# Optimization experiments

Hardware: AMD Instinct MI355X
Metric: run time of the kernel (lower is better)

Reference implementation:

```python
import jax, jax.numpy as jnp
import numpy as np

B, T, D, NH, L, E, K = 2, 1024, 512, 8, 4, 8, 2
H = D * 4
HD = D // NH
EPS = 1e-5
THETA = 10000.0
MOE_LAYERS = (0, 2)   # layer_idx % moe_freq == 0
DENSE_LAYERS = (1, 3)


def setup_inputs() -> dict:
    key = jax.random.key(0)
    ks = jax.random.split(key, 12)
    s = 0.02
    return {
        "x": jax.random.normal(ks[0], (B, T, D), jnp.float32),
        "qkv_w": jax.random.normal(ks[1], (L, 3 * D, D), jnp.float32) * s,
        "out_w": jax.random.normal(ks[2], (L, D, D), jnp.float32) * s,
        "norm1_w": jnp.ones((L, D), jnp.float32),
        "norm2_w": jnp.ones((L, D), jnp.float32),
        "router_w": jax.random.normal(ks[3], (2, E, D), jnp.float32) * s,
        "moe_w1": jax.random.normal(ks[4], (2, E, H, D), jnp.float32) * s,
        "moe_w2": jax.random.normal(ks[5], (2, E, D, H), jnp.float32) * s,
        "moe_w3": jax.random.normal(ks[6], (2, E, H, D), jnp.float32) * s,
        "f_w1": jax.random.normal(ks[7], (2, H, D), jnp.float32) * s,
        "f_w2": jax.random.normal(ks[8], (2, D, H), jnp.float32) * s,
        "f_w3": jax.random.normal(ks[9], (2, H, D), jnp.float32) * s,
        "norm_f": jnp.ones((D,), jnp.float32),
    }


def rmsnorm(x, w):
    return w * x * jax.lax.rsqrt(jnp.mean(x * x, axis=-1, keepdims=True) + EPS)


def rope_tables():
    inv_freq = 1.0 / (THETA ** (jnp.arange(0, HD, 2, dtype=jnp.float32) / HD))  # [HD/2]
    t = jnp.arange(T, dtype=jnp.float32)
    freqs = t[:, None] * inv_freq[None, :]  # [T, HD/2]
    return jnp.cos(freqs), jnp.sin(freqs)


def apply_rope(x, cos, sin):  # x: [B, NH, T, HD]
    x1, x2 = jnp.split(x, 2, axis=-1)
    return jnp.concatenate([x1 * cos - x2 * sin, x1 * sin + x2 * cos], axis=-1)


def attention(x, qkv_w, out_w, cos, sin, causal):
    qkv = x @ qkv_w.T  # [B, T, 3D]
    q, k, v = jnp.split(qkv, 3, axis=-1)
    sh = lambda a: a.reshape(B, T, NH, HD).transpose(0, 2, 1, 3)  # [B, NH, T, HD]
    q, k, v = sh(q), sh(k), sh(v)
    q = apply_rope(q, cos, sin)
    k = apply_rope(k, cos, sin)
    scores = jnp.einsum('bhqd,bhkd->bhqk', q, k) / np.sqrt(HD).astype(np.float32)
    scores = jnp.where(causal, scores, jnp.finfo(scores.dtype).min)
    attn = jax.nn.softmax(scores, axis=-1)
    out = jnp.einsum('bhqk,bhkd->bhqd', attn, v)
    out = out.transpose(0, 2, 1, 3).reshape(B, T, D)
    return out @ out_w.T


def swiglu(x, w1, w2, w3):
    return (jax.nn.silu(x @ w1.T) * (x @ w3.T)) @ w2.T


def moe(x, rw, w1, w2, w3):  # x: [N, D]
    n = x.shape[0]
    logits = x @ rw.T                              # [N, E]
    top_v, top_i = jax.lax.top_k(logits, K)        # [N, K]
    wts = jax.nn.softmax(top_v, axis=-1)           # [N, K]
    # combine[t, e] = sum_i wts[t, i] * 1[top_i[t, i] == e]
    combine = jnp.zeros((n, E), x.dtype).at[jnp.arange(n)[:, None], top_i].add(wts)
    gate = jax.nn.silu(jnp.einsum('nd,ehd->neh', x, w1))
    up = jnp.einsum('nd,ehd->neh', x, w3)
    expert_out = jnp.einsum('neh,edh->ned', gate * up, w2)  # [N, E, D]
    return jnp.einsum('ne,ned->nd', combine, expert_out)


def reference(x, qkv_w, out_w, norm1_w, norm2_w, router_w, moe_w1, moe_w2,
              moe_w3, f_w1, f_w2, f_w3, norm_f):
    cos, sin = rope_tables()
    causal = jnp.tril(jnp.ones((T, T), bool))
    h = x
    for l in range(L):
        h = h + attention(rmsnorm(h, norm1_w[l]), qkv_w[l], out_w[l], cos, sin, causal)
        hn = rmsnorm(h, norm2_w[l])
        if l in MOE_LAYERS:
            m = MOE_LAYERS.index(l)
            ff = moe(hn.reshape(-1, D), router_w[m], moe_w1[m], moe_w2[m], moe_w3[m]).reshape(B, T, D)
        else:
            m = DENSE_LAYERS.index(l)
            ff = swiglu(hn, f_w1[m], f_w2[m], f_w3[m])
        h = h + ff
    return rmsnorm(h, norm_f)
```

## Files before the change

### kernel.cpp

```cpp
#include <hip/hip_runtime.h>
#include <hip/hip_bf16.h>
#include <math.h>

#define Bc 2
#define Tc 1024
#define Dc 512
#define NHc 8
#define Lc 4
#define Ec 8
#define Kc 2
#define Hc 2048
#define HDc 64
#define Nc (Bc * Tc)
#define NKc (Nc * Kc)

typedef __bf16 bf16x8 __attribute__((ext_vector_type(8)));
typedef float  f32x4  __attribute__((ext_vector_type(4)));
typedef unsigned short ushort8v __attribute__((ext_vector_type(8)));

__device__ inline unsigned short f2bf(float f) {
    union { float f; unsigned u; } v; v.f = f;
    unsigned r = v.u + 0x7FFFu + ((v.u >> 16) & 1u);
    return (unsigned short)(r >> 16);
}
__device__ inline float bf2f(unsigned short b) {
    union { unsigned u; float f; } v; v.u = ((unsigned)b) << 16;
    return v.f;
}
__device__ inline void splitbf(float a, unsigned short& hi, unsigned short& lo) {
    unsigned short h = f2bf(a);
    hi = h;
    lo = f2bf(a - bf2f(h));
}
__device__ inline void split8(const float4& a, const float4& b,
                              ushort8v& h, ushort8v& l) {
    unsigned short hh, ll;
    splitbf(a.x, hh, ll); h[0] = hh; l[0] = ll;
    splitbf(a.y, hh, ll); h[1] = hh; l[1] = ll;
    splitbf(a.z, hh, ll); h[2] = hh; l[2] = ll;
    splitbf(a.w, hh, ll); h[3] = hh; l[3] = ll;
    splitbf(b.x, hh, ll); h[4] = hh; l[4] = ll;
    splitbf(b.y, hh, ll); h[5] = hh; l[5] = ll;
    splitbf(b.z, hh, ll); h[6] = hh; l[6] = ll;
    splitbf(b.w, hh, ll); h[7] = hh; l[7] = ll;
}

__global__ __launch_bounds__(256) void rmsnorm_kernel(
    const float* __restrict__ x, const float* __restrict__ w,
    float* __restrict__ y)
{
    int row = blockIdx.x;
    const float* xr = x + (size_t)row * Dc;
    __shared__ float red[256];
    int tid = threadIdx.x;
    float ss = 0.0f;
    for (int d = tid; d < Dc; d += 256) { float v = xr[d]; ss += v * v; }
    red[tid] = ss; __syncthreads();
    for (int s = 128; s > 0; s >>= 1) {
        if (tid < s) red[tid] += red[tid + s];
        __syncthreads();
    }
    float inv = rsqrtf(red[0] / (float)Dc + 1e-5f);
    for (int d = tid; d < Dc; d += 256)
        y[(size_t)row * Dc + d] = w[d] * xr[d] * inv;
}

template<int MODE, int TM, int TN>
__global__ __launch_bounds__(256) void gemm3(
    const float* __restrict__ A, const float* __restrict__ Wbase,
    float* __restrict__ C, int M, int N, int K,
    const int* __restrict__ tok, const float* __restrict__ twt,
    const int* __restrict__ counts, const int* __restrict__ offsets,
    size_t wstride)
{
    constexpr int PAD = 40;
    constexpr int PA  = TM / 64;
    constexpr int PB  = TN / 64;
    constexpr int FM  = TM / 32;
    constexpr int FN  = TN / 32;

    int e = (MODE == 5) ? blockIdx.z : 0;
    int count = M, offs = 0;
    if (MODE == 5) {
        count = counts[e];
        offs  = offsets[e];
        if ((int)(blockIdx.y * TM) >= count) return;
    }
    const float* W = Wbase + (size_t)e * wstride;

    __shared__ __align__(16) unsigned short Ah[TM][PAD];
    __shared__ __align__(16) unsigned short Al[TM][PAD];
    __shared__ __align__(16) unsigned short Bh[TN][PAD];
    __shared__ __align__(16) unsigned short Bl[TN][PAD];

    int tid = threadIdx.x;
    int m0 = blockIdx.y * TM, n0 = blockIdx.x * TN;
    int srow = tid >> 2;
    int scol = (tid & 3) * 8;

    int wave = tid >> 6, lane = tid & 63;
    int wm = wave >> 1, wn = wave & 1;
    int quad = lane >> 4, l16 = lane & 15;

    f32x4 acc[FM][FN];
#pragma unroll
    for (int mi = 0; mi < FM; ++mi)
#pragma unroll
        for (int ni = 0; ni < FN; ++ni)
            acc[mi][ni] = (f32x4){0.f, 0.f, 0.f, 0.f};

    size_t arow[PA];
#pragma unroll
    for (int p = 0; p < PA; ++p) {
        int row = p * 64 + srow;
        if (MODE == 5) {
            int rr = m0 + row; if (rr >= count) rr = 0;
            arow[p] = (size_t)(offs + rr) * K;
        } else {
            arow[p] = (size_t)(m0 + row) * K;
        }
    }
    size_t brow[PB];
#pragma unroll
    for (int p = 0; p < PB; ++p)
        brow[p] = (size_t)(n0 + p * 64 + srow) * K;

    float4 pa[PA][2], pb[PB][2];
#pragma unroll
    for (int p = 0; p < PA; ++p) {
        pa[p][0] = *(const float4*)(A + arow[p] + scol);
        pa[p][1] = *(const float4*)(A + arow[p] + scol + 4);
    }
#pragma unroll
    for (int p = 0; p < PB; ++p) {
        pb[p][0] = *(const float4*)(W + brow[p] + scol);
        pb[p][1] = *(const float4*)(W + brow[p] + scol + 4);
    }

    for (int k0 = 0; k0 < K; k0 += 32) {
#pragma unroll
        for (int p = 0; p < PA; ++p) {
            int row = p * 64 + srow;
            ushort8v h, l;
            split8(pa[p][0], pa[p][1], h, l);
            *(ushort8v*)&Ah[row][scol] = h;
            *(ushort8v*)&Al[row][scol] = l;
        }
#pragma unroll
        for (int p = 0; p < PB; ++p) {
            int row = p * 64 + srow;
            ushort8v h, l;
            split8(pb[p][0], pb[p][1], h, l);
            *(ushort8v*)&Bh[row][scol] = h;
            *(ushort8v*)&Bl[row][scol] = l;
        }
        __syncthreads();
        if (k0 + 32 < K) {
            int kn = k0 + 32;
#pragma unroll
            for (int p = 0; p < PA; ++p) {
                pa[p][0] = *(const float4*)(A + arow[p] + kn + scol);
                pa[p][1] = *(const float4*)(A + arow[p] + kn + scol + 4);
            }
#pragma unroll
            for (int p = 0; p < PB; ++p) {
                pb[p][0] = *(const float4*)(W + brow[p] + kn + scol);
                pb[p][1] = *(const float4*)(W + brow[p] + kn + scol + 4);
            }
        }

        bf16x8 ah[FM], al[FM], bh[FN], bl[FN];
#pragma unroll
        for (int mi = 0; mi < FM; ++mi) {
            ah[mi] = *(const bf16x8*)&Ah[wm * (TM / 2) + mi * 16 + l16][quad * 8];
            al[mi] = *(const bf16x8*)&Al[wm * (TM / 2) + mi * 16 + l16][quad * 8];
        }
#pragma unroll
        for (int ni = 0; ni < FN; ++ni) {
            bh[ni] = *(const bf16x8*)&Bh[wn * (TN / 2) + ni * 16 + l16][quad * 8];
            bl[ni] = *(const bf16x8*)&Bl[wn * (TN / 2) + ni * 16 + l16][quad * 8];
        }
#pragma unroll
        for (int mi = 0; mi < FM; ++mi)
#pragma unroll
            for (int ni = 0; ni < FN; ++ni) {
                acc[mi][ni] = __builtin_amdgcn_mfma_f32_16x16x32_bf16(
                    ah[mi], bh[ni], acc[mi][ni], 0, 0, 0);
                acc[mi][ni] = __builtin_amdgcn_mfma_f32_16x16x32_bf16(
                    al[mi], bh[ni], acc[mi][ni], 0, 0, 0);
                acc[mi][ni] = __builtin_amdgcn_mfma_f32_16x16x32_bf16(
                    ah[mi], bl[ni], acc[mi][ni], 0, 0, 0);
            }
        __syncthreads();
    }

#pragma unroll
    for (int mi = 0; mi < FM; ++mi) {
#pragma unroll
        for (int ni = 0; ni < FN; ++ni) {
            int col = n0 + wn * (TN / 2) + ni * 16 + l16;
#pragma unroll
            for (int r = 0; r < 4; ++r) {
                int row = wm * (TM / 2) + mi * 16 + quad * 4 + r;
                float v = acc[mi][ni][r];
                if (MODE == 0) {
                    C[(size_t)(m0 + row) * N + col] = v;
                } else if (MODE == 1) {
                    C[(size_t)(m0 + row) * N + col] += v;
                } else {
                    int rr = m0 + row;
                    if (rr < count) {
                        int dest = tok[offs + rr];
                        float w = twt[offs + rr];
                        atomicAdd(&C[(size_t)dest * N + col], w * v);
                    }
                }
            }
        }
    }
}

template<bool GATHER>
__global__ __launch_bounds__(256) void ffn_fused(
    const float* __restrict__ A, const float* __restrict__ W1base,
    const float* __restrict__ W3base, float* __restrict__ T,
    int M, int N, int K,
    const int* __restrict__ tok, const int* __restrict__ counts,
    const int* __restrict__ offsets, size_t wstride)
{
    constexpr int TM = 64, TN = 128, PAD = 40;
    constexpr int FM = 2, FN = 4;

    int e = GATHER ? blockIdx.z : 0;
    int count = M, offs = 0;
    if (GATHER) {
        count = counts[e];
        offs  = offsets[e];
        if ((int)(blockIdx.y * TM) >= count) return;
    }
    const float* W1 = W1base + (size_t)e * wstride;
    const float* W3 = W3base + (size_t)e * wstride;

    __shared__ __align__(16) unsigned short Ah[TM][PAD];
    __shared__ __align__(16) unsigned short Al[TM][PAD];
    __shared__ __align__(16) unsigned short B1h[TN][PAD];
    __shared__ __align__(16) unsigned short B1l[TN][PAD];
    __shared__ __align__(16) unsigned short B3h[TN][PAD];
    __shared__ __align__(16) unsigned short B3l[TN][PAD];
    __shared__ int sTok[TM];

    int tid = threadIdx.x;
    int m0 = blockIdx.y * TM, n0 = blockIdx.x * TN;

    if (GATHER) {
        if (tid < TM) {
            int r = m0 + tid;
            sTok[tid] = (r < count) ? tok[offs + r] : tok[offs];
        }
        __syncthreads();
    }

    int srow = tid >> 2;
    int scol = (tid & 3) * 8;
    int wave = tid >> 6, lane = tid & 63;
    int wm = wave >> 1, wn = wave & 1;
    int quad = lane >> 4, l16 = lane & 15;

    f32x4 accg[FM][FN], accu[FM][FN];
#pragma unroll
    for (int mi = 0; mi < FM; ++mi)
#pragma unroll
        for (int ni = 0; ni < FN; ++ni) {
            accg[mi][ni] = (f32x4){0.f, 0.f, 0.f, 0.f};
            accu[mi][ni] = (f32x4){0.f, 0.f, 0.f, 0.f};
        }

    size_t arow;
    if (GATHER) arow = (size_t)sTok[srow] * K;
    else        arow = (size_t)(m0 + srow) * K;
    size_t brow[2];
    brow[0] = (size_t)(n0 + srow) * K;
    brow[1] = (size_t)(n0 + 64 + srow) * K;

    float4 pa[2], p1[2][2], p3[2][2];
    pa[0] = *(const float4*)(A + arow + scol);
    pa[1] = *(const float4*)(A + arow + scol + 4);
#pragma unroll
    for (int p = 0; p < 2; ++p) {
        p1[p][0] = *(const float4*)(W1 + brow[p] + scol);
        p1[p][1] = *(const float4*)(W1 + brow[p] + scol + 4);
        p3[p][0] = *(const float4*)(W3 + brow[p] + scol);
        p3[p][1] = *(const float4*)(W3 + brow[p] + scol + 4);
    }

    for (int k0 = 0; k0 < K; k0 += 32) {
        {
            ushort8v h, l;
            split8(pa[0], pa[1], h, l);
            *(ushort8v*)&Ah[srow][scol] = h;
            *(ushort8v*)&Al[srow][scol] = l;
        }
#pragma unroll
        for (int p = 0; p < 2; ++p) {
            int row = p * 64 + srow;
            ushort8v h, l;
            split8(p1[p][0], p1[p][1], h, l);
            *(ushort8v*)&B1h[row][scol] = h;
            *(ushort8v*)&B1l[row][scol] = l;
            split8(p3[p][0], p3[p][1], h, l);
            *(ushort8v*)&B3h[row][scol] = h;
            *(ushort8v*)&B3l[row][scol] = l;
        }
        __syncthreads();
        if (k0 + 32 < K) {
            int kn = k0 + 32;
            pa[0] = *(const float4*)(A + arow + kn + scol);
            pa[1] = *(const float4*)(A + arow + kn + scol + 4);
#pragma unroll
            for (int p = 0; p < 2; ++p) {
                p1[p][0] = *(const float4*)(W1 + brow[p] + kn + scol);
                p1[p][1] = *(const float4*)(W1 + brow[p] + kn + scol + 4);
                p3[p][0] = *(const float4*)(W3 + brow[p] + kn + scol);
                p3[p][1] = *(const float4*)(W3 + brow[p] + kn + scol + 4);
            }
        }

        bf16x8 ah[FM], al[FM], bh[FN], bl[FN];
#pragma unroll
        for (int mi = 0; mi < FM; ++mi) {
            ah[mi] = *(const bf16x8*)&Ah[wm * 32 + mi * 16 + l16][quad * 8];
            al[mi] = *(const bf16x8*)&Al[wm * 32 + mi * 16 + l16][quad * 8];
        }
#pragma unroll
        for (int ni = 0; ni < FN; ++ni) {
            bh[ni] = *(const bf16x8*)&B1h[wn * 64 + ni * 16 + l16][quad * 8];
            bl[ni] = *(const bf16x8*)&B1l[wn * 64 + ni * 16 + l16][quad * 8];
        }
#pragma unroll
        for (int mi = 0; mi < FM; ++mi)
#pragma unroll
            for (int ni = 0; ni < FN; ++ni) {
                accg[mi][ni] = __builtin_amdgcn_mfma_f32_16x16x32_bf16(
                    ah[mi], bh[ni], accg[mi][ni], 0, 0, 0);
                accg[mi][ni] = __builtin_amdgcn_mfma_f32_16x16x32_bf16(
                    al[mi], bh[ni], accg[mi][ni], 0, 0, 0);
                accg[mi][ni] = __builtin_amdgcn_mfma_f32_16x16x32_bf16(
                    ah[mi], bl[ni], accg[mi][ni], 0, 0, 0);
            }
#pragma unroll
        for (int ni = 0; ni < FN; ++ni) {
            bh[ni] = *(const bf16x8*)&B3h[wn * 64 + ni * 16 + l16][quad * 8];
            bl[ni] = *(const bf16x8*)&B3l[wn * 64 + ni * 16 + l16][quad * 8];
        }
#pragma unroll
        for (int mi = 0; mi < FM; ++mi)
#pragma unroll
            for (int ni = 0; ni < FN; ++ni) {
                accu[mi][ni] = __builtin_amdgcn_mfma_f32_16x16x32_bf16(
                    ah[mi], bh[ni], accu[mi][ni], 0, 0, 0);
                accu[mi][ni] = __builtin_amdgcn_mfma_f32_16x16x32_bf16(
                    al[mi], bh[ni], accu[mi][ni], 0, 0, 0);
                accu[mi][ni] = __builtin_amdgcn_mfma_f32_16x16x32_bf16(
                    ah[mi], bl[ni], accu[mi][ni], 0, 0, 0);
            }
        __syncthreads();
    }

#pragma unroll
    for (int mi = 0; mi < FM; ++mi) {
#pragma unroll
        for (int ni = 0; ni < FN; ++ni) {
            int col = n0 + wn * 64 + ni * 16 + l16;
#pragma unroll
            for (int r = 0; r < 4; ++r) {
                int row = wm * 32 + mi * 16 + quad * 4 + r;
                float g = accg[mi][ni][r];
                float u = accu[mi][ni][r];
                float t = (g / (1.0f + expf(-g))) * u;
                if (GATHER) {
                    int rr = m0 + row;
                    if (rr < count) T[(size_t)(offs + rr) * N + col] = t;
                } else {
                    T[(size_t)(m0 + row) * N + col] = t;
                }
            }
        }
    }
}

__global__ __launch_bounds__(256) void rope_kernel(float* __restrict__ qkv)
{
    const int HD2 = HDc / 2;
    int idx = blockIdx.x * blockDim.x + threadIdx.x;
    int total = Nc * NHc * HD2;
    if (idx >= total) return;
    int i = idx % HD2;
    int hh = (idx / HD2) % NHc;
    int n = idx / (HD2 * NHc);
    int t = n % Tc;
    float invf = expf(-(2.0f * (float)i / (float)HDc) * logf(10000.0f));
    float f = (float)t * invf;
    float c = cosf(f), s = sinf(f);
    size_t base = (size_t)n * (3 * Dc) + (size_t)hh * HDc;
    float* qp = qkv + base;
    float* kp = qkv + base + Dc;
    float q1 = qp[i], q2 = qp[i + HD2];
    qp[i]       = q1 * c - q2 * s;
    qp[i + HD2] = q1 * s + q2 * c;
    float k1 = kp[i], k2 = kp[i + HD2];
    kp[i]       = k1 * c - k2 * s;
    kp[i + HD2] = k1 * s + k2 * c;
}

__global__ __launch_bounds__(256) void attn_mfma(
    const float* __restrict__ qkv, float* __restrict__ out)
{
    constexpr int PAD = 72;
    __shared__ __align__(16) unsigned short Qh[64][PAD];
    __shared__ __align__(16) unsigned short Ql[64][PAD];
    __shared__ __align__(16) unsigned short Kh[64][PAD];
    __shared__ __align__(16) unsigned short Kl[64][PAD];
    __shared__ __align__(16) unsigned short Vth[64][PAD];
    __shared__ __align__(16) unsigned short Vtl[64][PAD];

    int qb = blockIdx.x, bh = blockIdx.y;
    int b = bh >> 3, hh = bh & 7;
    const int D3 = 3 * Dc;
    const float* base = qkv + (size_t)b * Tc * D3 + (size_t)hh * HDc;

    int tid = threadIdx.x;
    int wave = tid >> 6, lane = tid & 63;
    int quad = lane >> 4, l16 = lane & 15;

    int srow = tid >> 2;
    int scb  = (tid & 3) * 16;
    int vhd  = lane;
    int vkb  = wave * 16;

    {
        const float* qp = base + (size_t)(qb * 64 + srow) * D3 + scb;
        float4 q0 = *(const float4*)(qp);
        float4 q1 = *(const float4*)(qp + 4);
        float4 q2 = *(const float4*)(qp + 8);
        float4 q3 = *(const float4*)(qp + 12);
        const float sc = 0.125f;
        q0.x *= sc; q0.y *= sc; q0.z *= sc; q0.w *= sc;
        q1.x *= sc; q1.y *= sc; q1.z *= sc; q1.w *= sc;
        q2.x *= sc; q2.y *= sc; q2.z *= sc; q2.w *= sc;
        q3.x *= sc; q3.y *= sc; q3.z *= sc; q3.w *= sc;
        ushort8v h, l;
        split8(q0, q1, h, l);
        *(ushort8v*)&Qh[srow][scb]     = h;
        *(ushort8v*)&Ql[srow][scb]     = l;
        split8(q2, q3, h, l);
        *(ushort8v*)&Qh[srow][scb + 8] = h;
        *(ushort8v*)&Ql[srow][scb + 8] = l;
    }
    __syncthreads();
    bf16x8 qah[2], qal[2];
#pragma unroll
    for (int ks = 0; ks < 2; ++ks) {
        qah[ks] = *(const bf16x8*)&Qh[wave * 16 + l16][ks * 32 + quad * 8];
        qal[ks] = *(const bf16x8*)&Ql[wave * 16 + l16][ks * 32 + quad * 8];
    }

    float4 kf0, kf1, kf2, kf3;
    float vf[16];
    {
        const float* kp = base + (size_t)srow * D3 + Dc + scb;
        kf0 = *(const float4*)(kp);
        kf1 = *(const float4*)(kp + 4);
        kf2 = *(const float4*)(kp + 8);
        kf3 = *(const float4*)(kp + 12);
        const float* vp = base + (size_t)vkb * D3 + 2 * Dc + vhd;
#pragma unroll
        for (int i = 0; i < 16; ++i) vf[i] = vp[(size_t)i * D3];
    }

    f32x4 o[4];
#pragma unroll
    for (int f = 0; f < 4; ++f) o[f] = (f32x4){0.f, 0.f, 0.f, 0.f};
    float mrow[4], lrow[4];
#pragma unroll
    for (int r = 0; r < 4; ++r) { mrow[r] = -1e30f; lrow[r] = 0.0f; }

    for (int kt = 0; kt <= qb; ++kt) {
        __syncthreads();
        {
            ushort8v h, l;
            split8(kf0, kf1, h, l);
            *(ushort8v*)&Kh[srow][scb]     = h;
            *(ushort8v*)&Kl[srow][scb]     = l;
            split8(kf2, kf3, h, l);
            *(ushort8v*)&Kh[srow][scb + 8] = h;
            *(ushort8v*)&Kl[srow][scb + 8] = l;
        }
        {
            float4 v0 = make_float4(vf[0], vf[1], vf[2], vf[3]);
            float4 v1 = make_float4(vf[4], vf[5], vf[6], vf[7]);
            float4 v2 = make_float4(vf[8], vf[9], vf[10], vf[11]);
            float4 v3 = make_float4(vf[12], vf[13], vf[14], vf[15]);
            ushort8v h, l;
            split8(v0, v1, h, l);
            *(ushort8v*)&Vth[vhd][vkb]     = h;
            *(ushort8v*)&Vtl[vhd][vkb]     = l;
            split8(v2, v3, h, l);
            *(ushort8v*)&Vth[vhd][vkb + 8] = h;
            *(ushort8v*)&Vtl[vhd][vkb + 8] = l;
        }
        __syncthreads();
        if (kt < qb) {
            const float* kp = base + (size_t)((kt + 1) * 64 + srow) * D3 + Dc + scb;
            kf0 = *(const float4*)(kp);
            kf1 = *(const float4*)(kp + 4);
            kf2 = *(const float4*)(kp + 8);
            kf3 = *(const float4*)(kp + 12);
            const float* vp = base + (size_t)((kt + 1) * 64 + vkb) * D3 + 2 * Dc + vhd;
#pragma unroll
            for (int i = 0; i < 16; ++i) vf[i] = vp[(size_t)i * D3];
        }

        f32x4 s[4];
#pragma unroll
        for (int ni = 0; ni < 4; ++ni) s[ni] = (f32x4){0.f, 0.f, 0.f, 0.f};
#pragma unroll
        for (int ks = 0; ks < 2; ++ks) {
            bf16x8 kh_[4], kl_[4];
#pragma unroll
            for (int ni = 0; ni < 4; ++ni) {
                kh_[ni] = *(const bf16x8*)&Kh[ni * 16 + l16][ks * 32 + quad * 8];
                kl_[ni] = *(const bf16x8*)&Kl[ni * 16 + l16][ks * 32 + quad * 8];
            }
#pragma unroll
            for (int ni = 0; ni < 4; ++ni) {
                s[ni] = __builtin_amdgcn_mfma_f32_16x16x32_bf16(
                    qah[ks], kh_[ni], s[ni], 0, 0, 0);
                s[ni] = __builtin_amdgcn_mfma_f32_16x16x32_bf16(
                    qal[ks], kh_[ni], s[ni], 0, 0, 0);
                s[ni] = __builtin_amdgcn_mfma_f32_16x16x32_bf16(
                    qah[ks], kl_[ni], s[ni], 0, 0, 0);
            }
        }

        if (kt == qb) {
#pragma unroll
            for (int ni = 0; ni < 4; ++ni)
#pragma unroll
                for (int r = 0; r < 4; ++r)
                    if (ni * 16 + l16 > wave * 16 + quad * 4 + r)
                        s[ni][r] = -1e30f;
        }

        float al4[4];
#pragma unroll
        for (int r = 0; r < 4; ++r) {
            float rm = fmaxf(fmaxf(s[0][r], s[1][r]), fmaxf(s[2][r], s[3][r]));
            rm = fmaxf(rm, __shfl_xor(rm, 1));
            rm = fmaxf(rm, __shfl_xor(rm, 2));
            rm = fmaxf(rm, __shfl_xor(rm, 4));
            rm = fmaxf(rm, __shfl_xor(rm, 8));
            float mn = fmaxf(mrow[r], rm);
            al4[r] = __expf(mrow[r] - mn);
            mrow[r] = mn;
            float rs = 0.0f;
#pragma unroll
            for (int ni = 0; ni < 4; ++ni) {
                float pv = __expf(s[ni][r] - mn);
                s[ni][r] = pv;
                rs += pv;
            }
            rs += __shfl_xor(rs, 1);
            rs += __shfl_xor(rs, 2);
            rs += __shfl_xor(rs, 4);
            rs += __shfl_xor(rs, 8);
            lrow[r] = lrow[r] * al4[r] + rs;
        }

        __syncthreads();
#pragma unroll
        for (int ni = 0; ni < 4; ++ni)
#pragma unroll
            for (int r = 0; r < 4; ++r) {
                unsigned short hp, lp;
                splitbf(s[ni][r], hp, lp);
                Kh[wave * 16 + quad * 4 + r][ni * 16 + l16] = hp;
                Kl[wave * 16 + quad * 4 + r][ni * 16 + l16] = lp;
            }
#pragma unroll
        for (int f = 0; f < 4; ++f)
#pragma unroll
            for (int r = 0; r < 4; ++r)
                o[f][r] *= al4[r];
#pragma unroll
        for (int ks = 0; ks < 2; ++ks) {
            bf16x8 pah = *(const bf16x8*)&Kh[wave * 16 + l16][ks * 32 + quad * 8];
            bf16x8 pal = *(const bf16x8*)&Kl[wave * 16 + l16][ks * 32 + quad * 8];
#pragma unroll
            for (int f = 0; f < 4; ++f) {
                bf16x8 vh_ = *(const bf16x8*)&Vth[f * 16 + l16][ks * 32 + quad * 8];
                bf16x8 vl_ = *(const bf16x8*)&Vtl[f * 16 + l16][ks * 32 + quad * 8];
                o[f] = __builtin_amdgcn_mfma_f32_16x16x32_bf16(
                    pah, vh_, o[f], 0, 0, 0);
                o[f] = __builtin_amdgcn_mfma_f32_16x16x32_bf16(
                    pal, vh_, o[f], 0, 0, 0);
                o[f] = __builtin_amdgcn_mfma_f32_16x16x32_bf16(
                    pah, vl_, o[f], 0, 0, 0);
            }
        }
    }

#pragma unroll
    for (int r = 0; r < 4; ++r) {
        float inv = 1.0f / lrow[r];
        int q = qb * 64 + wave * 16 + quad * 4 + r;
#pragma unroll
        for (int f = 0; f < 4; ++f)
            out[(size_t)(b * Tc + q) * Dc + hh * HDc + f * 16 + l16] =
                o[f][r] * inv;
    }
}

__global__ __launch_bounds__(64) void router_kernel(
    const float* __restrict__ x, const float* __restrict__ rw,
    float* __restrict__ logits)
{
    int n = blockIdx.x;
    int lane = threadIdx.x;
    const float* xr = x + (size_t)n * Dc;
    for (int e = 0; e < Ec; ++e) {
        const float* wr = rw + (size_t)e * Dc;
        float p = 0.0f;
        for (int d = lane; d < Dc; d += 64) p += xr[d] * wr[d];
        for (int off = 32; off > 0; off >>= 1) p += __shfl_down(p, off);
        if (lane == 0) logits[(size_t)n * Ec + e] = p;
    }
}

__global__ void zero8_kernel(int* __restrict__ counts)
{
    if (threadIdx.x < Ec) counts[threadIdx.x] = 0;
}

__global__ __launch_bounds__(256) void topk_count_kernel(
    const float* __restrict__ logits, int* __restrict__ counts,
    int2* __restrict__ eidx, float2* __restrict__ ewt)
{
    int n = blockIdx.x * blockDim.x + threadIdx.x;
    if (n >= Nc) return;
    const float* lg = logits + (size_t)n * Ec;
    int i0 = -1, i1 = -1;
    float v0 = -1e30f, v1 = -1e30f;
    for (int e = 0; e < Ec; ++e) {
        float v = lg[e];
        if (v > v0) { v1 = v0; i1 = i0; v0 = v; i0 = e; }
        else if (v > v1) { v1 = v; i1 = e; }
    }
    float e1 = expf(v1 - v0);
    float w0 = 1.0f / (1.0f + e1);
    float w1 = e1 / (1.0f + e1);
    atomicAdd(&counts[i0], 1);
    atomicAdd(&counts[i1], 1);
    eidx[n] = make_int2(i0, i1);
    ewt[n]  = make_float2(w0, w1);
}

__global__ void scan_kernel(int* __restrict__ counts, int* __restrict__ offsets)
{
    if (threadIdx.x == 0) {
        int s = 0;
        for (int e = 0; e < Ec; ++e) { offsets[e] = s; s += counts[e]; counts[e] = 0; }
    }
}

__global__ __launch_bounds__(256) void topk_place_kernel(
    const int2* __restrict__ eidx, const float2* __restrict__ ewt,
    int* __restrict__ counts, const int* __restrict__ offsets,
    int* __restrict__ tok, float* __restrict__ twt)
{
    int n = blockIdx.x * blockDim.x + threadIdx.x;
    if (n >= Nc) return;
    int2 ei = eidx[n];
    float2 w = ewt[n];
    int p0 = atomicAdd(&counts[ei.x], 1);
    int r0 = offsets[ei.x] + p0;
    tok[r0] = n; twt[r0] = w.x;
    int p1 = atomicAdd(&counts[ei.y], 1);
    int r1 = offsets[ei.y] + p1;
    tok[r1] = n; twt[r1] = w.y;
}

extern "C" void kernel_launch(void* const* d_in, const int* in_sizes, int n_in,
                              void* d_out, int out_size, void* d_ws, size_t ws_size,
                              hipStream_t stream)
{
    const float* x        = (const float*)d_in[0];
    const float* qkv_w    = (const float*)d_in[1];
    const float* out_w    = (const float*)d_in[2];
    const float* norm1_w  = (const float*)d_in[3];
    const float* norm2_w  = (const float*)d_in[4];
    const float* router_w = (const float*)d_in[5];
    const float* moe_w1   = (const float*)d_in[6];
    const float* moe_w2   = (const float*)d_in[7];
    const float* moe_w3   = (const float*)d_in[8];
    const float* f_w1     = (const float*)d_in[9];
    const float* f_w2     = (const float*)d_in[10];
    const float* f_w3     = (const float*)d_in[11];
    const float* norm_f   = (const float*)d_in[12];
    float* out = (float*)d_out;

    float* p = (float*)d_ws;
    float* h      = p;  p += Nc * Dc;
    float* xn     = p;  p += Nc * Dc;
    float* arena  = p;  p += (size_t)NKc * Hc;
    float* logits = p;  p += Nc * Ec;
    int*   counts  = (int*)p;  p += 16;
    int*   offsets = (int*)p;  p += 16;
    int2*  eidx    = (int2*)p; p += 2 * Nc;
    float* ewt     = p;        p += 2 * Nc;
    int*   tok     = (int*)p;  p += NKc;
    float* twt     = p;        p += NKc;

    float* qkv  = arena;
    float* attn = xn;
    float* t    = arena;

    hipMemcpyAsync(h, x, (size_t)Nc * Dc * sizeof(float),
                   hipMemcpyDeviceToDevice, stream);

    for (int l = 0; l < Lc; ++l) {
        rmsnorm_kernel<<<Nc, 256, 0, stream>>>(h, norm1_w + (size_t)l * Dc, xn);
        gemm3<0, 64, 128><<<dim3(3 * Dc / 128, Nc / 64, 1), 256, 0, stream>>>(
            xn, qkv_w + (size_t)l * 3 * Dc * Dc, qkv, Nc, 3 * Dc, Dc,
            nullptr, nullptr, nullptr, nullptr, 0);
        {
            int total = Nc * NHc * (HDc / 2);
            rope_kernel<<<(total + 255) / 256, 256, 0, stream>>>(qkv);
        }
        attn_mfma<<<dim3(Tc / 64, Bc * NHc), 256, 0, stream>>>(qkv, attn);
        gemm3<1, 64, 64><<<dim3(Dc / 64, Nc / 64, 1), 256, 0, stream>>>(
            attn, out_w + (size_t)l * Dc * Dc, h, Nc, Dc, Dc,
            nullptr, nullptr, nullptr, nullptr, 0);

        rmsnorm_kernel<<<Nc, 256, 0, stream>>>(h, norm2_w + (size_t)l * Dc, xn);
        if (l == 0 || l == 2) {
            int m = l / 2;
            router_kernel<<<Nc, 64, 0, stream>>>(
                xn, router_w + (size_t)m * Ec * Dc, logits);
            zero8_kernel<<<1, 64, 0, stream>>>(counts);
            topk_count_kernel<<<Nc / 256, 256, 0, stream>>>(
                logits, counts, eidx, (float2*)ewt);
            scan_kernel<<<1, 64, 0, stream>>>(counts, offsets);
            topk_place_kernel<<<Nc / 256, 256, 0, stream>>>(
                eidx, (float2*)ewt, counts, offsets, tok, twt);

            ffn_fused<true><<<dim3(Hc / 128, NKc / 64, Ec), 256, 0, stream>>>(
                xn, moe_w1 + (size_t)m * Ec * Hc * Dc,
                moe_w3 + (size_t)m * Ec * Hc * Dc, t, Nc, Hc, Dc,
                tok, counts, offsets, (size_t)Hc * Dc);
            gemm3<5, 64, 64><<<dim3(Dc / 64, NKc / 64, Ec), 256, 0, stream>>>(
                t, moe_w2 + (size_t)m * Ec * Dc * Hc, h, Nc, Dc, Hc,
                tok, twt, counts, offsets, (size_t)Dc * Hc);
        } else {
            int m = (l - 1) / 2;
            ffn_fused<false><<<dim3(Hc / 128, Nc / 64, 1), 256, 0, stream>>>(
                xn, f_w1 + (size_t)m * Hc * Dc, f_w3 + (size_t)m * Hc * Dc,
                t, Nc, Hc, Dc, nullptr, nullptr, nullptr, 0);
            gemm3<1, 64, 64><<<dim3(Dc / 64, Nc / 64, 1), 256, 0, stream>>>(
                t, f_w2 + (size_t)m * Dc * Hc, h, Nc, Dc, Hc,
                nullptr, nullptr, nullptr, nullptr, 0);
        }
    }

    rmsnorm_kernel<<<Nc, 256, 0, stream>>>(h, norm_f, out);
}
```

Baseline: 1.413 ms.

## Pre-split weights and activations into bf16 hi/lo arrays before GEMMs

Adds a split_w kernel that converts each fp32 weight matrix into separate bf16 hi and lo arrays before use. The rmsnorm, attention and FFN epilogues now also write their outputs as hi/lo bf16 pairs. The GEMM kernels then load the pre-split operands directly instead of converting fp32 tiles inside the k-loop. This removes redundant per-tile split arithmetic, which was repeated across every block that reads the same tile, at the cost of extra launches and an extra full pass over all weights on every call.

```diff
diff --git a/kernel.cpp b/kernel.cpp
--- a/kernel.cpp
+++ b/kernel.cpp
@@ -17,6 +17,7 @@
 typedef __bf16 bf16x8 __attribute__((ext_vector_type(8)));
 typedef float  f32x4  __attribute__((ext_vector_type(4)));
 typedef unsigned short ushort8v __attribute__((ext_vector_type(8)));
+typedef unsigned short ushort4v __attribute__((ext_vector_type(4)));
 
 __device__ inline unsigned short f2bf(float f) {
     union { float f; unsigned u; } v; v.f = f;
@@ -45,9 +46,27 @@
     splitbf(b.w, hh, ll); h[7] = hh; l[7] = ll;
 }
 
-__global__ __launch_bounds__(256) void rmsnorm_kernel(
+__global__ __launch_bounds__(256) void split_w_kernel(
+    const float* __restrict__ w, unsigned short* __restrict__ hi,
+    unsigned short* __restrict__ lo, int n4)
+{
+    int i = blockIdx.x * 256 + threadIdx.x;
+    if (i >= n4) return;
+    float4 v = ((const float4*)w)[i];
+    ushort4v h, l;
+    unsigned short a, b;
+    splitbf(v.x, a, b); h[0] = a; l[0] = b;
+    splitbf(v.y, a, b); h[1] = a; l[1] = b;
+    splitbf(v.z, a, b); h[2] = a; l[2] = b;
+    splitbf(v.w, a, b); h[3] = a; l[3] = b;
+    ((ushort4v*)hi)[i] = h;
+    ((ushort4v*)lo)[i] = l;
+}
+
+__global__ __launch_bounds__(256) void rmsnorm_split_kernel(
     const float* __restrict__ x, const float* __restrict__ w,
-    float* __restrict__ y)
+    float* __restrict__ y, unsigned short* __restrict__ yh,
+    unsigned short* __restrict__ yl)
 {
     int row = blockIdx.x;
     const float* xr = x + (size_t)row * Dc;
@@ -61,13 +80,40 @@
         __syncthreads();
     }
     float inv = rsqrtf(red[0] / (float)Dc + 1e-5f);
+    for (int d = tid; d < Dc; d += 256) {
+        float v = w[d] * xr[d] * inv;
+        size_t idx = (size_t)row * Dc + d;
+        y[idx] = v;
+        unsigned short h, l;
+        splitbf(v, h, l);
+        yh[idx] = h; yl[idx] = l;
+    }
+}
+
+__global__ __launch_bounds__(256) void rmsnorm_kernel(
+    const float* __restrict__ x, const float* __restrict__ w,
+    float* __restrict__ y)
+{
+    int row = blockIdx.x;
+    const float* xr = x + (size_t)row * Dc;
+    __shared__ float red[256];
+    int tid = threadIdx.x;
+    float ss = 0.0f;
+    for (int d = tid; d < Dc; d += 256) { float v = xr[d]; ss += v * v; }
+    red[tid] = ss; __syncthreads();
+    for (int s = 128; s > 0; s >>= 1) {
+        if (tid < s) red[tid] += red[tid + s];
+        __syncthreads();
+    }
+    float inv = rsqrtf(red[0] / (float)Dc + 1e-5f);
     for (int d = tid; d < Dc; d += 256)
         y[(size_t)row * Dc + d] = w[d] * xr[d] * inv;
 }
 
 template<int MODE, int TM, int TN>
-__global__ __launch_bounds__(256) void gemm3(
-    const float* __restrict__ A, const float* __restrict__ Wbase,
+__global__ __launch_bounds__(256) void gemm3p(
+    const unsigned short* __restrict__ Ahi, const unsigned short* __restrict__ Alo,
+    const unsigned short* __restrict__ Whibase, const unsigned short* __restrict__ Wlobase,
     float* __restrict__ C, int M, int N, int K,
     const int* __restrict__ tok, const float* __restrict__ twt,
     const int* __restrict__ counts, const int* __restrict__ offsets,
@@ -86,7 +132,8 @@
         offs  = offsets[e];
         if ((int)(blockIdx.y * TM) >= count) return;
     }
-    const float* W = Wbase + (size_t)e * wstride;
+    const unsigned short* Whi = Whibase + (size_t)e * wstride;
+    const unsigned short* Wlo = Wlobase + (size_t)e * wstride;
 
     __shared__ __align__(16) unsigned short Ah[TM][PAD];
     __shared__ __align__(16) unsigned short Al[TM][PAD];
@@ -125,47 +172,43 @@
     for (int p = 0; p < PB; ++p)
         brow[p] = (size_t)(n0 + p * 64 + srow) * K;
 
-    float4 pa[PA][2], pb[PB][2];
+    ushort8v pah[PA], pal[PA], pbh[PB], pbl[PB];
 #pragma unroll
     for (int p = 0; p < PA; ++p) {
-        pa[p][0] = *(const float4*)(A + arow[p] + scol);
-        pa[p][1] = *(const float4*)(A + arow[p] + scol + 4);
+        pah[p] = *(const ushort8v*)(Ahi + arow[p] + scol);
+        pal[p] = *(const ushort8v*)(Alo + arow[p] + scol);
     }
 #pragma unroll
     for (int p = 0; p < PB; ++p) {
-        pb[p][0] = *(const float4*)(W + brow[p] + scol);
-        pb[p][1] = *(const float4*)(W + brow[p] + scol + 4);
+        pbh[p] = *(const ushort8v*)(Whi + brow[p] + scol);
+        pbl[p] = *(const ushort8v*)(Wlo + brow[p] + scol);
     }
 
     for (int k0 = 0; k0 < K; k0 += 32) {
 #pragma unroll
         for (int p = 0; p < PA; ++p) {
             int row = p * 64 + srow;
-            ushort8v h, l;
-            split8(pa[p][0], pa[p][1], h, l);
-            *(ushort8v*)&Ah[row][scol] = h;
-            *(ushort8v*)&Al[row][scol] = l;
+            *(ushort8v*)&Ah[row][scol] = pah[p];
+            *(ushort8v*)&Al[row][scol] = pal[p];
         }
 #pragma unroll
         for (int p = 0; p < PB; ++p) {
             int row = p * 64 + srow;
-            ushort8v h, l;
-            split8(pb[p][0], pb[p][1], h, l);
-            *(ushort8v*)&Bh[row][scol] = h;
-            *(ushort8v*)&Bl[row][scol] = l;
+            *(ushort8v*)&Bh[row][scol] = pbh[p];
+            *(ushort8v*)&Bl[row][scol] = pbl[p];
         }
         __syncthreads();
         if (k0 + 32 < K) {
             int kn = k0 + 32;
 #pragma unroll
             for (int p = 0; p < PA; ++p) {
-                pa[p][0] = *(const float4*)(A + arow[p] + kn + scol);
-                pa[p][1] = *(const float4*)(A + arow[p] + kn + scol + 4);
+                pah[p] = *(const ushort8v*)(Ahi + arow[p] + kn + scol);
+                pal[p] = *(const ushort8v*)(Alo + arow[p] + kn + scol);
             }
 #pragma unroll
             for (int p = 0; p < PB; ++p) {
-                pb[p][0] = *(const float4*)(W + brow[p] + kn + scol);
-                pb[p][1] = *(const float4*)(W + brow[p] + kn + scol + 4);
+                pbh[p] = *(const ushort8v*)(Whi + brow[p] + kn + scol);
+                pbl[p] = *(const ushort8v*)(Wlo + brow[p] + kn + scol);
             }
         }
 
@@ -221,9 +264,11 @@
 }
 
 template<bool GATHER>
-__global__ __launch_bounds__(256) void ffn_fused(
-    const float* __restrict__ A, const float* __restrict__ W1base,
-    const float* __restrict__ W3base, float* __restrict__ T,
+__global__ __launch_bounds__(256) void ffn_fusedp(
+    const unsigned short* __restrict__ Ahi, const unsigned short* __restrict__ Alo,
+    const unsigned short* __restrict__ W1hibase, const unsigned short* __restrict__ W1lobase,
+    const unsigned short* __restrict__ W3hibase, const unsigned short* __restrict__ W3lobase,
+    unsigned short* __restrict__ Thi, unsigned short* __restrict__ Tlo,
     int M, int N, int K,
     const int* __restrict__ tok, const int* __restrict__ counts,
     const int* __restrict__ offsets, size_t wstride)
@@ -238,8 +283,10 @@
         offs  = offsets[e];
         if ((int)(blockIdx.y * TM) >= count) return;
     }
-    const float* W1 = W1base + (size_t)e * wstride;
-    const float* W3 = W3base + (size_t)e * wstride;
+    const unsigned short* W1hi = W1hibase + (size_t)e * wstride;
+    const unsigned short* W1lo = W1lobase + (size_t)e * wstride;
+    const unsigned short* W3hi = W3hibase + (size_t)e * wstride;
+    const unsigned short* W3lo = W3lobase + (size_t)e * wstride;
 
     __shared__ __align__(16) unsigned short Ah[TM][PAD];
     __shared__ __align__(16) unsigned short Al[TM][PAD];
@@ -282,46 +329,39 @@
     brow[0] = (size_t)(n0 + srow) * K;
     brow[1] = (size_t)(n0 + 64 + srow) * K;
 
-    float4 pa[2], p1[2][2], p3[2][2];
-    pa[0] = *(const float4*)(A + arow + scol);
-    pa[1] = *(const float4*)(A + arow + scol + 4);
+    ushort8v pah, pal, p1h[2], p1l[2], p3h[2], p3l[2];
+    pah = *(const ushort8v*)(Ahi + arow + scol);
+    pal = *(const ushort8v*)(Alo + arow + scol);
 #pragma unroll
     for (int p = 0; p < 2; ++p) {
-        p1[p][0] = *(const float4*)(W1 + brow[p] + scol);
-        p1[p][1] = *(const float4*)(W1 + brow[p] + scol + 4);
-        p3[p][0] = *(const float4*)(W3 + brow[p] + scol);
-        p3[p][1] = *(const float4*)(W3 + brow[p] + scol + 4);
+        p1h[p] = *(const ushort8v*)(W1hi + brow[p] + scol);
+        p1l[p] = *(const ushort8v*)(W1lo + brow[p] + scol);
+        p3h[p] = *(const ushort8v*)(W3hi + brow[p] + scol);
+        p3l[p] = *(const ushort8v*)(W3lo + brow[p] + scol);
     }
 
     for (int k0 = 0; k0 < K; k0 += 32) {
-        {
-            ushort8v h, l;
-            split8(pa[0], pa[1], h, l);
-            *(ushort8v*)&Ah[srow][scol] = h;
-            *(ushort8v*)&Al[srow][scol] = l;
-        }
+        *(ushort8v*)&Ah[srow][scol] = pah;
+        *(ushort8v*)&Al[srow][scol] = pal;
 #pragma unroll
         for (int p = 0; p < 2; ++p) {
             int row = p * 64 + srow;
-            ushort8v h, l;
-            split8(p1[p][0], p1[p][1], h, l);
-            *(ushort8v*)&B1h[row][scol] = h;
-            *(ushort8v*)&B1l[row][scol] = l;
-            split8(p3[p][0], p3[p][1], h, l);
-            *(ushort8v*)&B3h[row][scol] = h;
-            *(ushort8v*)&B3l[row][scol] = l;
+            *(ushort8v*)&B1h[row][scol] = p1h[p];
+            *(ushort8v*)&B1l[row][scol] = p1l[p];
+            *(ushort8v*)&B3h[row][scol] = p3h[p];
+            *(ushort8v*)&B3l[row][scol] = p3l[p];
         }
         __syncthreads();
         if (k0 + 32 < K) {
             int kn = k0 + 32;
-            pa[0] = *(const float4*)(A + arow + kn + scol);
-            pa[1] = *(const float4*)(A + arow + kn + scol + 4);
+            pah = *(const ushort8v*)(Ahi + arow + kn + scol);
+            pal = *(const ushort8v*)(Alo + arow + kn + scol);
 #pragma unroll
             for (int p = 0; p < 2; ++p) {
-                p1[p][0] = *(const float4*)(W1 + brow[p] + kn + scol);
-                p1[p][1] = *(const float4*)(W1 + brow[p] + kn + scol + 4);
-                p3[p][0] = *(const float4*)(W3 + brow[p] + kn + scol);
-                p3[p][1] = *(const float4*)(W3 + brow[p] + kn + scol + 4);
+                p1h[p] = *(const ushort8v*)(W1hi + brow[p] + kn + scol);
+                p1l[p] = *(const ushort8v*)(W1lo + brow[p] + kn + scol);
+                p3h[p] = *(const ushort8v*)(W3hi + brow[p] + kn + scol);
+                p3l[p] = *(const ushort8v*)(W3lo + brow[p] + kn + scol);
             }
         }
 
@@ -377,11 +417,17 @@
                 float g = accg[mi][ni][r];
                 float u = accu[mi][ni][r];
                 float t = (g / (1.0f + expf(-g))) * u;
+                unsigned short th, tl;
+                splitbf(t, th, tl);
                 if (GATHER) {
                     int rr = m0 + row;
-                    if (rr < count) T[(size_t)(offs + rr) * N + col] = t;
+                    if (rr < count) {
+                        size_t idx = (size_t)(offs + rr) * N + col;
+                        Thi[idx] = th; Tlo[idx] = tl;
+                    }
                 } else {
-                    T[(size_t)(m0 + row) * N + col] = t;
+                    size_t idx = (size_t)(m0 + row) * N + col;
+                    Thi[idx] = th; Tlo[idx] = tl;
                 }
             }
         }
@@ -413,7 +459,8 @@
 }
 
 __global__ __launch_bounds__(256) void attn_mfma(
-    const float* __restrict__ qkv, float* __restrict__ out)
+    const float* __restrict__ qkv, unsigned short* __restrict__ outh,
+    unsigned short* __restrict__ outl)
 {
     constexpr int PAD = 72;
     __shared__ __align__(16) unsigned short Qh[64][PAD];
@@ -614,9 +661,12 @@
         float inv = 1.0f / lrow[r];
         int q = qb * 64 + wave * 16 + quad * 4 + r;
 #pragma unroll
-        for (int f = 0; f < 4; ++f)
-            out[(size_t)(b * Tc + q) * Dc + hh * HDc + f * 16 + l16] =
-                o[f][r] * inv;
+        for (int f = 0; f < 4; ++f) {
+            size_t idx = (size_t)(b * Tc + q) * Dc + hh * HDc + f * 16 + l16;
+            unsigned short hp, lp;
+            splitbf(o[f][r] * inv, hp, lp);
+            outh[idx] = hp; outl[idx] = lp;
+        }
     }
 }
 
@@ -711,6 +761,8 @@
     float* p = (float*)d_ws;
     float* h      = p;  p += Nc * Dc;
     float* xn     = p;  p += Nc * Dc;
+    unsigned short* xnh = (unsigned short*)p;  p += Nc * Dc / 2;
+    unsigned short* xnl = (unsigned short*)p;  p += Nc * Dc / 2;
     float* arena  = p;  p += (size_t)NKc * Hc;
     float* logits = p;  p += Nc * Ec;
     int*   counts  = (int*)p;  p += 16;
@@ -719,29 +771,49 @@
     float* ewt     = p;        p += 2 * Nc;
     int*   tok     = (int*)p;  p += NKc;
     float* twt     = p;        p += NKc;
-
-    float* qkv  = arena;
-    float* attn = xn;
-    float* t    = arena;
+    unsigned short* wqh = (unsigned short*)p;
+    unsigned short* wql = wqh + (size_t)3 * Dc * Dc;
+    unsigned short* woh = wql + (size_t)3 * Dc * Dc;
+    unsigned short* wol = woh + (size_t)Dc * Dc;
+    unsigned short* wah = wol + (size_t)Dc * Dc;
+    unsigned short* wal = wah + (size_t)Ec * Hc * Dc;
+    unsigned short* wbh = wal + (size_t)Ec * Hc * Dc;
+    unsigned short* wbl = wbh + (size_t)Ec * Hc * Dc;
+
+    float* qkv = arena;
+    unsigned short* th = (unsigned short*)arena;
+    unsigned short* tl = th + (size_t)NKc * Hc;
 
     hipMemcpyAsync(h, x, (size_t)Nc * Dc * sizeof(float),
                    hipMemcpyDeviceToDevice, stream);
 
     for (int l = 0; l < Lc; ++l) {
-        rmsnorm_kernel<<<Nc, 256, 0, stream>>>(h, norm1_w + (size_t)l * Dc, xn);
-        gemm3<0, 64, 128><<<dim3(3 * Dc / 128, Nc / 64, 1), 256, 0, stream>>>(
-            xn, qkv_w + (size_t)l * 3 * Dc * Dc, qkv, Nc, 3 * Dc, Dc,
+        {
+            int n4 = 3 * Dc * Dc / 4;
+            split_w_kernel<<<(n4 + 255) / 256, 256, 0, stream>>>(
+                qkv_w + (size_t)l * 3 * Dc * Dc, wqh, wql, n4);
+        }
+        rmsnorm_split_kernel<<<Nc, 256, 0, stream>>>(
+            h, norm1_w + (size_t)l * Dc, xn, xnh, xnl);
+        gemm3p<0, 64, 128><<<dim3(3 * Dc / 128, Nc / 64, 1), 256, 0, stream>>>(
+            xnh, xnl, wqh, wql, qkv, Nc, 3 * Dc, Dc,
             nullptr, nullptr, nullptr, nullptr, 0);
         {
             int total = Nc * NHc * (HDc / 2);
             rope_kernel<<<(total + 255) / 256, 256, 0, stream>>>(qkv);
         }
-        attn_mfma<<<dim3(Tc / 64, Bc * NHc), 256, 0, stream>>>(qkv, attn);
-        gemm3<1, 64, 64><<<dim3(Dc / 64, Nc / 64, 1), 256, 0, stream>>>(
-            attn, out_w + (size_t)l * Dc * Dc, h, Nc, Dc, Dc,
+        {
+            int n4 = Dc * Dc / 4;
+            split_w_kernel<<<(n4 + 255) / 256, 256, 0, stream>>>(
+                out_w + (size_t)l * Dc * Dc, woh, wol, n4);
+        }
+        attn_mfma<<<dim3(Tc / 64, Bc * NHc), 256, 0, stream>>>(qkv, xnh, xnl);
+        gemm3p<1, 64, 64><<<dim3(Dc / 64, Nc / 64, 1), 256, 0, stream>>>(
+            xnh, xnl, woh, wol, h, Nc, Dc, Dc,
             nullptr, nullptr, nullptr, nullptr, 0);
 
-        rmsnorm_kernel<<<Nc, 256, 0, stream>>>(h, norm2_w + (size_t)l * Dc, xn);
+        rmsnorm_split_kernel<<<Nc, 256, 0, stream>>>(
+            h, norm2_w + (size_t)l * Dc, xn, xnh, xnl);
         if (l == 0 || l == 2) {
             int m = l / 2;
             router_kernel<<<Nc, 64, 0, stream>>>(
@@ -753,20 +825,33 @@
             topk_place_kernel<<<Nc / 256, 256, 0, stream>>>(
                 eidx, (float2*)ewt, counts, offsets, tok, twt);
 
-            ffn_fused<true><<<dim3(Hc / 128, NKc / 64, Ec), 256, 0, stream>>>(
-                xn, moe_w1 + (size_t)m * Ec * Hc * Dc,
-                moe_w3 + (size_t)m * Ec * Hc * Dc, t, Nc, Hc, Dc,
+            int n4 = Ec * Hc * Dc / 4;
+            split_w_kernel<<<(n4 + 255) / 256, 256, 0, stream>>>(
+                moe_w1 + (size_t)m * Ec * Hc * Dc, wah, wal, n4);
+            split_w_kernel<<<(n4 + 255) / 256, 256, 0, stream>>>(
+                moe_w3 + (size_t)m * Ec * Hc * Dc, wbh, wbl, n4);
+            ffn_fusedp<true><<<dim3(Hc / 128, NKc / 64, Ec), 256, 0, stream>>>(
+                xnh, xnl, wah, wal, wbh, wbl, th, tl, Nc, Hc, Dc,
                 tok, counts, offsets, (size_t)Hc * Dc);
-            gemm3<5, 64, 64><<<dim3(Dc / 64, NKc / 64, Ec), 256, 0, stream>>>(
-                t, moe_w2 + (size_t)m * Ec * Dc * Hc, h, Nc, Dc, Hc,
+            split_w_kernel<<<(n4 + 255) / 256, 256, 0, stream>>>(
+                moe_w2 + (size_t)m * Ec * Dc * Hc, wah, wal, n4);
+            gemm3p<5, 64, 64><<<dim3(Dc / 64, NKc / 64, Ec), 256, 0, stream>>>(
+                th, tl, wah, wal, h, Nc, Dc, Hc,
                 tok, twt, counts, offsets, (size_t)Dc * Hc);
         } else {
             int m = (l - 1) / 2;
-            ffn_fused<false><<<dim3(Hc / 128, Nc / 64, 1), 256, 0, stream>>>(
-                xn, f_w1 + (size_t)m * Hc * Dc, f_w3 + (size_t)m * Hc * Dc,
-                t, Nc, Hc, Dc, nullptr, nullptr, nullptr, 0);
-            gemm3<1, 64, 64><<<dim3(Dc / 64, Nc / 64, 1), 256, 0, stream>>>(
-                t, f_w2 + (size_t)m * Dc * Hc, h, Nc, Dc, Hc,
+            int n4 = Hc * Dc / 4;
+            split_w_kernel<<<(n4 + 255) / 256, 256, 0, stream>>>(
+                f_w1 + (size_t)m * Hc * Dc, wah, wal, n4);
+            split_w_kernel<<<(n4 + 255) / 256, 256, 0, stream>>>(
+                f_w3 + (size_t)m * Hc * Dc, wbh, wbl, n4);
+            ffn_fusedp<false><<<dim3(Hc / 128, Nc / 64, 1), 256, 0, stream>>>(
+                xnh, xnl, wah, wal, wbh, wbl, th, tl, Nc, Hc, Dc,
+                nullptr, nullptr, nullptr, 0);
+            split_w_kernel<<<(n4 + 255) / 256, 256, 0, stream>>>(
+                f_w2 + (size_t)m * Dc * Hc, wah, wal, n4);
+            gemm3p<1, 64, 64><<<dim3(Dc / 64, Nc / 64, 1), 256, 0, stream>>>(
+                th, tl, wah, wal, h, Nc, Dc, Hc,
                 nullptr, nullptr, nullptr, nullptr, 0);
         }
     }
```

After: 1.382 ms. -2.2%, faster.
